# Optimization experiments

Measured on AMD Instinct MI355X. Metric: run time of the kernel, lower is better.

Reference implementation:

```python
import jax, jax.numpy as jnp
from jax import lax
import numpy as np

NDIM = 256
BATCH = 65536
NROT = NDIM * (NDIM - 1) // 2  # comb(ndim, 2) = 32640


def _givens_mat(rots, ii, jj, ndim):
    """Product G_last @ ... @ G_1 of Givens rotations in combinations order.

    Left-multiplying by G(i, j, theta) only modifies rows i and j, so we apply
    each rotation as a rank-2 row update instead of a full matmul (same math
    as the original `plane_rot_mat @ mat` loop).
    """
    def step(mat, carry):
        i, j, th = carry
        c = jnp.cos(th)
        s = jnp.sin(th)
        ri = mat[i]
        rj = mat[j]
        mat = mat.at[i].set(c * ri - s * rj)
        mat = mat.at[j].set(s * ri + c * rj)
        return mat, None

    mat0 = jnp.eye(ndim, dtype=jnp.complex64)
    mat, _ = lax.scan(step, mat0, (ii, jj, rots))
    return mat


def setup_inputs() -> dict:
    key = jax.random.key(0)
    k1, k2, k3, k4 = jax.random.split(key, 4)
    x = jax.random.normal(k1, (BATCH, NDIM), dtype=jnp.float32)
    rots1 = 0.1 * jax.random.normal(k2, (NROT,), dtype=jnp.float32)
    phases = 0.1 * jax.random.normal(k3, (NDIM,), dtype=jnp.float32)
    rots2 = 0.1 * jax.random.normal(k4, (NROT,), dtype=jnp.float32)
    return {"x": x, "rots1": rots1, "phases": phases, "rots2": rots2}


def reference(x, rots1, phases, rots2):
    ndim = x.shape[1]
    # np.triu_indices(ndim, 1) enumerates (i, j) pairs in the same row-major
    # order as itertools.combinations(range(ndim), 2).
    ii_np, jj_np = np.triu_indices(ndim, k=1)
    ii = jnp.asarray(ii_np, dtype=jnp.int32)
    jj = jnp.asarray(jj_np, dtype=jnp.int32)

    # vector_norm: row-wise L2 normalization
    xn = x / jnp.linalg.norm(x, axis=1, keepdims=True)
    xc = xn.astype(jnp.complex64)

    # rot1: y = x @ M1.T with M1 = G_last @ ... @ G_1
    M1 = _givens_mat(rots1, ii, jj, ndim)
    y = xc @ M1.T

    # phase_transforms: x @ diag(exp(i*phases)) == elementwise phase multiply
    y = y * jnp.exp(1j * phases)

    # rot2
    M2 = _givens_mat(rots2, ii, jj, ndim)
    y = y @ M2.T

    # measure: |.|^2
    return jnp.abs(y) ** 2
```

## Files before the change

### kernel.cpp

```cpp
#include <hip/hip_runtime.h>
#include <stdint.h>
#include <math.h>

#define NDIM 256
#define BATCH 65536
#define NROT 32640

typedef float  f32x4 __attribute__((ext_vector_type(4)));
typedef short  s16x8 __attribute__((ext_vector_type(8)));
typedef unsigned int u32x4 __attribute__((ext_vector_type(4)));
typedef unsigned int u32x2 __attribute__((ext_vector_type(2)));

static __device__ __forceinline__ unsigned short f2bf(float f) {
    unsigned int u = __float_as_uint(f);
    u += 0x7fffu + ((u >> 16) & 1u);
    return (unsigned short)(u >> 16);
}
static __device__ __forceinline__ float bf2f(unsigned short h) {
    return __uint_as_float(((unsigned)h) << 16);
}

static __device__ __forceinline__ void split4(f32x4 v, u32x2* hi, u32x2* lo) {
    unsigned short h[4], l[4];
    #pragma unroll
    for (int i = 0; i < 4; i++) {
        h[i] = f2bf(v[i]);
        l[i] = f2bf(v[i] - bf2f(h[i]));
    }
    *hi = (u32x2){ (unsigned)h[0] | ((unsigned)h[1] << 16),
                   (unsigned)h[2] | ((unsigned)h[3] << 16) };
    *lo = (u32x2){ (unsigned)l[0] | ((unsigned)l[1] << 16),
                   (unsigned)l[2] | ((unsigned)l[3] << 16) };
}
static __device__ __forceinline__ void split8(const float* v, u32x4* hi, u32x4* lo) {
    unsigned short h[8], l[8];
    #pragma unroll
    for (int i = 0; i < 8; i++) {
        h[i] = f2bf(v[i]);
        l[i] = f2bf(v[i] - bf2f(h[i]));
    }
    *hi = (u32x4){ (unsigned)h[0] | ((unsigned)h[1] << 16),
                   (unsigned)h[2] | ((unsigned)h[3] << 16),
                   (unsigned)h[4] | ((unsigned)h[5] << 16),
                   (unsigned)h[6] | ((unsigned)h[7] << 16) };
    *lo = (u32x4){ (unsigned)l[0] | ((unsigned)l[1] << 16),
                   (unsigned)l[2] | ((unsigned)l[3] << 16),
                   (unsigned)l[4] | ((unsigned)l[5] << 16),
                   (unsigned)l[6] | ((unsigned)l[7] << 16) };
}

static __device__ __forceinline__ int sweep_bound(int k, int pblk) {
    int target = k * (NROT / pblk);
    int best = 0, bd = 0x7fffffff;
    for (int i = 0; i <= 256; i += 4) {
        int pre = i * 255 - (i * (i - 1)) / 2;
        int d = pre - target; d = (d < 0) ? -d : d;
        if (d < bd) { bd = d; best = i; }
    }
    return best;
}

__global__ __launch_bounds__(256) void k_cs(const float* __restrict__ r1,
                                            const float* __restrict__ r2,
                                            float2* __restrict__ cs) {
    int i = blockIdx.x * 256 + threadIdx.x;
    float th = (i < NROT) ? r1[i] : r2[i - NROT];
    float sv, cv; sincosf(th, &sv, &cv);
    cs[i] = make_float2(cv, sv);
}

__global__ __launch_bounds__(64) void k_blocks(const float2* __restrict__ cs,
                                               float* __restrict__ bmats, int pblk) {
    __shared__ float colb[264 * 64];
    __shared__ float2 csb[256 * 4];
    __shared__ float2 tri[24 * 6];

    const int t = threadIdx.x;
    const int bid = blockIdx.x;
    const int chunk = bid & 3;
    const int b = (bid >> 2) % pblk;
    const int set = (bid >> 2) / pblk;
    const int col0 = chunk * 64;
    const float2* cst = cs + (size_t)set * NROT;

    const int s0 = sweep_bound(b, pblk);
    const int s1 = sweep_bound(b + 1, pblk);
    const int ngroups = (s1 - s0) >> 2;

    {
        const f32x4 z = {0.f, 0.f, 0.f, 0.f};
        #pragma unroll 11
        for (int q = 0; q < 66; q++)
            *(f32x4*)&colb[(q * 64 + t) * 4] = z;
        colb[(col0 + t) * 64 + t] = 1.0f;
    }

    for (int k = t; k < ngroups * 6; k += 64) {
        int g = k / 6, q = k - g * 6;
        int a  = (q < 3) ? 0 : ((q < 5) ? 1 : 2);
        int bb = (q < 3) ? (q + 1) : ((q < 5) ? (q - 1) : 3);
        int m0 = s0 + g * 4;
        int m = m0 + a;
        int base = m * 255 - (m * (m - 1)) / 2;
        tri[k] = cst[base - m - 1 + m0 + bb];
    }

    float2 gv[16];
    {
        const int m0g = s0;
        int offg[4];
        #pragma unroll
        for (int a = 0; a < 4; a++) {
            int m = m0g + a;
            offg[a] = m * 255 - (m * (m - 1)) / 2 - m - 1;
        }
        #pragma unroll
        for (int it = 0; it < 16; it++) {
            int k = t + it * 64;
            int jj = k >> 2, a = k & 3;
            int j = m0g + 4 + jj;
            gv[it] = (j < 256) ? cst[offg[a] + j] : make_float2(1.f, 0.f);
        }
        #pragma unroll
        for (int it = 0; it < 16; it++)
            csb[t + it * 64] = gv[it];
    }

    for (int g = 0; g < ngroups; g++) {
        const int m0 = s0 + g * 4;
        const int n_j = 252 - m0;
        const int n_p = (n_j > 0) ? ((n_j + 7) & ~7) : 0;
        const float* csbuf = (const float*)&csb[0];

        const bool have_next = (g + 1 < ngroups);
        if (have_next) {
            const int m0g = m0 + 4;
            int offg[4];
            #pragma unroll
            for (int a = 0; a < 4; a++) {
                int m = m0g + a;
                offg[a] = m * 255 - (m * (m - 1)) / 2 - m - 1;
            }
            #pragma unroll
            for (int it = 0; it < 16; it++) {
                int k = t + it * 64;
                int jj = k >> 2, a = k & 3;
                int j = m0g + 4 + jj;
                gv[it] = (j < 256) ? cst[offg[a] + j] : make_float2(1.f, 0.f);
            }
        }

        float u0 = colb[(m0 + 0) * 64 + t];
        float u1 = colb[(m0 + 1) * 64 + t];
        float u2 = colb[(m0 + 2) * 64 + t];
        float u3 = colb[(m0 + 3) * 64 + t];

        {
            float2 cv; float nr;
            cv = tri[g * 6 + 0]; nr = cv.y * u0 + cv.x * u1; u0 = cv.x * u0 - cv.y * u1; u1 = nr;
            cv = tri[g * 6 + 1]; nr = cv.y * u0 + cv.x * u2; u0 = cv.x * u0 - cv.y * u2; u2 = nr;
            cv = tri[g * 6 + 2]; nr = cv.y * u0 + cv.x * u3; u0 = cv.x * u0 - cv.y * u3; u3 = nr;
            cv = tri[g * 6 + 3]; nr = cv.y * u1 + cv.x * u2; u1 = cv.x * u1 - cv.y * u2; u2 = nr;
            cv = tri[g * 6 + 4]; nr = cv.y * u1 + cv.x * u3; u1 = cv.x * u1 - cv.y * u3; u3 = nr;
            cv = tri[g * 6 + 5]; nr = cv.y * u2 + cv.x * u3; u2 = cv.x * u2 - cv.y * u3; u3 = nr;
        }

        if (n_p > 0) {
            float rbuf[8];
            f32x4 abuf[8][2];
            #pragma unroll
            for (int p = 0; p < 8; p++) {
                rbuf[p] = colb[(m0 + 4 + p) * 64 + t];
                abuf[p][0] = *(const f32x4*)&csbuf[p * 8 + 0];
                abuf[p][1] = *(const f32x4*)&csbuf[p * 8 + 4];
            }
            for (int c = 0; c < n_p; c += 8) {
                #pragma unroll
                for (int p = 0; p < 8; p++) {
                    const int j = m0 + 4 + c + p;
                    float r = rbuf[p];
                    f32x4 A01 = abuf[p][0], A23 = abuf[p][1];
                    int jn = j + 8; jn = (jn < 263) ? jn : 263;
                    int cn = c + p + 8; cn = (cn < n_p) ? cn : (n_p - 1);
                    rbuf[p] = colb[jn * 64 + t];
                    abuf[p][0] = *(const f32x4*)&csbuf[cn * 8 + 0];
                    abuf[p][1] = *(const f32x4*)&csbuf[cn * 8 + 4];
                    float nr;
                    nr = A01[1] * u0 + A01[0] * r; u0 = A01[0] * u0 - A01[1] * r; r = nr;
                    nr = A01[3] * u1 + A01[2] * r; u1 = A01[2] * u1 - A01[3] * r; r = nr;
                    nr = A23[1] * u2 + A23[0] * r; u2 = A23[0] * u2 - A23[1] * r; r = nr;
                    nr = A23[3] * u3 + A23[2] * r; u3 = A23[2] * u3 - A23[3] * r; r = nr;
                    colb[j * 64 + t] = r;
                }
            }
        }
        colb[(m0 + 0) * 64 + t] = u0;
        colb[(m0 + 1) * 64 + t] = u1;
        colb[(m0 + 2) * 64 + t] = u2;
        colb[(m0 + 3) * 64 + t] = u3;

        if (have_next) {
            #pragma unroll
            for (int it = 0; it < 16; it++)
                csb[t + it * 64] = gv[it];
        }
    }

    float* outm = bmats + (size_t)(set * pblk + b) * 65536;
    for (int r = 0; r < 256; r++)
        outm[(size_t)r * 256 + col0 + t] = colb[r * 64 + t];
}

static __device__ __forceinline__ void xnorm_item(const float* __restrict__ xg,
                                                  unsigned short* __restrict__ xbf,
                                                  int id, int tid) {
    const int w = tid >> 6, lane = tid & 63;
    const int r0 = id * 64;
    #pragma unroll 2
    for (int p = 0; p < 16; p++) {
        int row = r0 + p * 4 + w;
        f32x4 v = *(const f32x4*)&xg[(size_t)row * 256 + lane * 4];
        float s = v[0] * v[0] + v[1] * v[1] + v[2] * v[2] + v[3] * v[3];
        #pragma unroll
        for (int off = 32; off; off >>= 1) s += __shfl_xor(s, off, 64);
        float sc = 1.0f / sqrtf(s);
        unsigned short h0 = f2bf(v[0] * sc), h1 = f2bf(v[1] * sc);
        unsigned short h2 = f2bf(v[2] * sc), h3 = f2bf(v[3] * sc);
        u32x2 pk = { (unsigned)h0 | ((unsigned)h1 << 16),
                     (unsigned)h2 | ((unsigned)h3 << 16) };
        *(u32x2*)&xbf[(size_t)row * 256 + lane * 4] = pk;
    }
}

#define TB 2560

static __device__ __forceinline__ int bslot(int row, int s) {
    return row * 40 + ((s ^ ((row >> 3) & 3)) << 3);
}

static __device__ __forceinline__ void tile_issueA(const float* __restrict__ Am,
                                                   int tr, int kb, int tid,
                                                   f32x4 va[2]) {
    #pragma unroll
    for (int it = 0; it < 2; it++) {
        int flat = tid + it * 256;
        int r = flat >> 3, c4 = flat & 7;
        va[it] = *(const f32x4*)&Am[(size_t)(tr * 64 + r) * 256 + kb * 32 + c4 * 4];
    }
}
static __device__ __forceinline__ void tile_issueB(const float* __restrict__ Bm,
                                                   int tc, int kb, int bn, int bkq,
                                                   float vb[8]) {
    #pragma unroll
    for (int i = 0; i < 8; i++)
        vb[i] = Bm[(size_t)(kb * 32 + bkq * 8 + i) * 256 + tc * 64 + bn];
}
static __device__ __forceinline__ void tile_commit(unsigned short* __restrict__ Ahi,
                                                   unsigned short* __restrict__ Alo,
                                                   unsigned short* __restrict__ Bhi,
                                                   unsigned short* __restrict__ Blo,
                                                   int tid, int bn, int bkq,
                                                   const f32x4 va[2], const float vb[8]) {
    #pragma unroll
    for (int it = 0; it < 2; it++) {
        int flat = tid + it * 256;
        int r = flat >> 3, c4 = flat & 7;
        u32x2 hi, lo; split4(va[it], &hi, &lo);
        *(u32x2*)&Ahi[r * 40 + c4 * 4] = hi;
        *(u32x2*)&Alo[r * 40 + c4 * 4] = lo;
    }
    u32x4 hi8, lo8; split8(vb, &hi8, &lo8);
    *(u32x4*)&Bhi[bslot(bn, bkq)] = hi8;
    *(u32x4*)&Blo[bslot(bn, bkq)] = lo8;
}
static __device__ __forceinline__ void tile_mfma(const unsigned short* __restrict__ Ahi,
                                                 const unsigned short* __restrict__ Alo,
                                                 const unsigned short* __restrict__ Bhi,
                                                 const unsigned short* __restrict__ Blo,
                                                 int mh, int nh, int l15, int lq,
                                                 f32x4 acc[2][2]) {
    s16x8 ah[2], al[2], bh[2], bl[2];
    #pragma unroll
    for (int tm = 0; tm < 2; tm++) {
        ah[tm] = *(const s16x8*)&Ahi[(mh + tm * 16 + l15) * 40 + lq * 8];
        al[tm] = *(const s16x8*)&Alo[(mh + tm * 16 + l15) * 40 + lq * 8];
    }
    #pragma unroll
    for (int tn = 0; tn < 2; tn++) {
        bh[tn] = *(const s16x8*)&Bhi[bslot(nh + tn * 16 + l15, lq)];
        bl[tn] = *(const s16x8*)&Blo[bslot(nh + tn * 16 + l15, lq)];
    }
    #pragma unroll
    for (int tm = 0; tm < 2; tm++)
        #pragma unroll
        for (int tn = 0; tn < 2; tn++) {
            acc[tm][tn] = __builtin_amdgcn_mfma_f32_16x16x32_bf16(ah[tm], bh[tn], acc[tm][tn], 0, 0, 0);
            acc[tm][tn] = __builtin_amdgcn_mfma_f32_16x16x32_bf16(ah[tm], bl[tn], acc[tm][tn], 0, 0, 0);
            acc[tm][tn] = __builtin_amdgcn_mfma_f32_16x16x32_bf16(al[tm], bh[tn], acc[tm][tn], 0, 0, 0);
        }
}

static __device__ void combine_tile(const float* __restrict__ src,
                                    float* __restrict__ dst,
                                    int half, int pblk, int bx, int by, int tid,
                                    unsigned short* Ahi, unsigned short* Alo,
                                    unsigned short* Bhi, unsigned short* Blo) {
    const int set = by / half, pidx = by % half;
    const int stride = pblk / (2 * half);
    const int s0A = sweep_bound((2 * pidx + 1) * stride, pblk);
    const float* Am = src + (size_t)(set * 2 * half + 2 * pidx + 1) * 65536;
    const float* Bm = src + (size_t)(set * 2 * half + 2 * pidx) * 65536;
    float* Dm = dst + (size_t)(set * half + pidx) * 65536;
    const int tr = bx >> 2, tc = bx & 3;

    if (tr * 64 + 64 <= s0A) {
        #pragma unroll
        for (int it = 0; it < 4; it++) {
            int flat = tid + it * 256;
            int r = flat >> 4, c4 = flat & 15;
            size_t idx = (size_t)(tr * 64 + r) * 256 + tc * 64 + c4 * 4;
            *(f32x4*)&Dm[idx] = *(const f32x4*)&Bm[idx];
        }
        return;
    }
    const int kb0 = (tr * 64 >= s0A) ? (s0A >> 5) : 0;

    const int lane = tid & 63, w = tid >> 6;
    const int mh = (w >> 1) * 32, nh = (w & 1) * 32;
    const int l15 = lane & 15, lq = lane >> 4;
    const int bn = tid & 63, bkq = tid >> 6;

    f32x4 acc[2][2];
    #pragma unroll
    for (int i = 0; i < 2; i++)
        #pragma unroll
        for (int j = 0; j < 2; j++) acc[i][j] = (f32x4){0.f, 0.f, 0.f, 0.f};

    f32x4 vaE[2], vaO[2]; float vbE[8], vbO[8];
    tile_issueA(Am, tr, kb0, tid, vaE);
    tile_issueB(Bm, tc, kb0, bn, bkq, vbE);
    if (kb0 + 1 < 8) {
        tile_issueA(Am, tr, kb0 + 1, tid, vaO);
        tile_issueB(Bm, tc, kb0 + 1, bn, bkq, vbO);
    }

    for (int kb = kb0; kb < 8; kb++) {
        const int cur = (kb - kb0) & 1;
        if (cur == 0) {
            tile_commit(Ahi, Alo, Bhi, Blo, tid, bn, bkq, vaE, vbE);
            __syncthreads();
            if (kb + 2 < 8) {
                tile_issueA(Am, tr, kb + 2, tid, vaE);
                tile_issueB(Bm, tc, kb + 2, bn, bkq, vbE);
            }
        } else {
            tile_commit(Ahi, Alo, Bhi, Blo, tid, bn, bkq, vaO, vbO);
            __syncthreads();
            if (kb + 2 < 8) {
                tile_issueA(Am, tr, kb + 2, tid, vaO);
                tile_issueB(Bm, tc, kb + 2, bn, bkq, vbO);
            }
        }
        tile_mfma(Ahi, Alo, Bhi, Blo, mh, nh, l15, lq, acc);
        __syncthreads();
    }
    #pragma unroll
    for (int tm = 0; tm < 2; tm++)
        #pragma unroll
        for (int tn = 0; tn < 2; tn++)
            #pragma unroll
            for (int r = 0; r < 4; r++)
                Dm[(size_t)(tr * 64 + mh + tm * 16 + lq * 4 + r) * 256
                   + tc * 64 + nh + tn * 16 + l15] = acc[tm][tn][r];
}

__global__ __launch_bounds__(256) void k_combine(const float* __restrict__ src,
                                                 float* __restrict__ dst,
                                                 int half, int pblk,
                                                 const float* __restrict__ xg,
                                                 unsigned short* __restrict__ xbf) {
    __shared__ unsigned short Ahi[TB], Alo[TB], Bhi[TB], Blo[TB];
    const int by = blockIdx.y, tid = threadIdx.x;
    if (by >= 2 * half) {
        xnorm_item(xg, xbf, (by - 2 * half) * 16 + blockIdx.x, tid);
        return;
    }
    combine_tile(src, dst, half, pblk, blockIdx.x, by, tid, Ahi, Alo, Bhi, Blo);
}

__global__ __launch_bounds__(256) void k_abt_part(const float* __restrict__ mats,
                                                  const float* __restrict__ phases,
                                                  float* __restrict__ part) {
    __shared__ unsigned short Ahi[TB], Alo[TB], Bhi[TB], Blo[TB];
    const float* Am = mats + 65536;
    const float* Bm = mats;
    const int tid = threadIdx.x;
    const int bx = blockIdx.x;
    const int v  = blockIdx.y;
    const int kb = blockIdx.z;
    const int tr = bx >> 2, tc = bx & 3;

    const int lane = tid & 63, w = tid >> 6;
    const int mh = (w >> 1) * 32, nh = (w & 1) * 32;
    const int l15 = lane & 15, lq = lane >> 4;
    const int bn = tid & 63, bkq = tid >> 6;

    f32x4 va[2]; float vb[8];
    tile_issueA(Am, tr, kb, tid, va);
    #pragma unroll
    for (int i = 0; i < 8; i++) {
        int kg = kb * 32 + bkq * 8 + i;
        float ph = phases[kg];
        float sc = v ? sinf(ph) : cosf(ph);
        vb[i] = Bm[(size_t)kg * 256 + tc * 64 + bn] * sc;
    }

    f32x4 acc[2][2];
    #pragma unroll
    for (int i = 0; i < 2; i++)
        #pragma unroll
        for (int j = 0; j < 2; j++) acc[i][j] = (f32x4){0.f, 0.f, 0.f, 0.f};

    tile_commit(Ahi, Alo, Bhi, Blo, tid, bn, bkq, va, vb);
    __syncthreads();
    tile_mfma(Ahi, Alo, Bhi, Blo, mh, nh, l15, lq, acc);

    float* pp = part + (size_t)(kb * 2 + v) * 65536;
    #pragma unroll
    for (int tm = 0; tm < 2; tm++)
        #pragma unroll
        for (int tn = 0; tn < 2; tn++)
            #pragma unroll
            for (int r = 0; r < 4; r++)
                pp[(size_t)(tr * 64 + mh + tm * 16 + lq * 4 + r) * 256
                   + tc * 64 + nh + tn * 16 + l15] = acc[tm][tn][r];
}

__global__ __launch_bounds__(256) void k_abt_red(const float* __restrict__ part,
                                                 unsigned short* __restrict__ abt) {
    const int e = (blockIdx.x * 256 + threadIdx.x) * 4;
    f32x4 s = {0.f, 0.f, 0.f, 0.f};
    #pragma unroll
    for (int kz = 0; kz < 8; kz++)
        s += *(const f32x4*)&part[(size_t)kz * 131072 + e];
    unsigned short h0 = f2bf(s[0]), h1 = f2bf(s[1]);
    unsigned short h2 = f2bf(s[2]), h3 = f2bf(s[3]);
    u32x2 pk = { (unsigned)h0 | ((unsigned)h1 << 16),
                 (unsigned)h2 | ((unsigned)h3 << 16) };
    *(u32x2*)&abt[e] = pk;
}

__global__ __launch_bounds__(256) void k_norm(const float* __restrict__ x,
                                              float* __restrict__ invn) {
    const int row = blockIdx.x * 4 + (threadIdx.x >> 6);
    const int lane = threadIdx.x & 63;
    f32x4 v = *(const f32x4*)&x[(size_t)row * 256 + lane * 4];
    float s = v[0] * v[0] + v[1] * v[1] + v[2] * v[2] + v[3] * v[3];
    for (int off = 32; off; off >>= 1) s += __shfl_xor(s, off, 64);
    if (lane == 0) invn[row] = 1.0f / sqrtf(s);
}

#define BKP 136
__global__ __launch_bounds__(256) void k_gemm_bf(const unsigned short* __restrict__ xbf,
                                                 const unsigned short* __restrict__ abt,
                                                 float* __restrict__ out) {
    __shared__ unsigned short As[128 * BKP];
    __shared__ unsigned short Bs[128 * BKP];
    const int tid = threadIdx.x;
    const int l  = blockIdx.y * 4 + blockIdx.x;
    const int L  = (l & 7) * 256 + (l >> 3);
    const int cb = L & 3;
    const int rb = L >> 2;
    const int lane = tid & 63, w = tid >> 6;

    f32x4 acc[16];
    #pragma unroll
    for (int i = 0; i < 16; i++) acc[i] = (f32x4){0.f, 0.f, 0.f, 0.f};

    int rA[8], cA[8], grB[8];
    #pragma unroll
    for (int it = 0; it < 8; it++) {
        int flat = tid + it * 256;
        rA[it] = flat >> 4; cA[it] = flat & 15;
        int r = rA[it];
        grB[it] = (r < 64) ? (cb * 64 + r) : (256 + cb * 64 + (r - 64));
    }

    u32x4 pa[8], pb[8];
    #pragma unroll
    for (int it = 0; it < 8; it++) {
        pa[it] = *(const u32x4*)&xbf[(size_t)(rb * 128 + rA[it]) * 256 + cA[it] * 8];
        pb[it] = *(const u32x4*)&abt[(size_t)grB[it] * 256 + cA[it] * 8];
    }
    #pragma unroll
    for (int it = 0; it < 8; it++) {
        *(u32x4*)&As[rA[it] * BKP + cA[it] * 8] = pa[it];
        *(u32x4*)&Bs[rA[it] * BKP + cA[it] * 8] = pb[it];
    }
    __syncthreads();
    #pragma unroll
    for (int it = 0; it < 8; it++) {
        pa[it] = *(const u32x4*)&xbf[(size_t)(rb * 128 + rA[it]) * 256 + 128 + cA[it] * 8];
        pb[it] = *(const u32x4*)&abt[(size_t)grB[it] * 256 + 128 + cA[it] * 8];
    }

    auto compute = [&]() {
        #pragma unroll
        for (int ks = 0; ks < 4; ks++) {
            const int k0 = ks * 32 + (lane >> 4) * 8;
            s16x8 a[2], b[8];
            #pragma unroll
            for (int tm = 0; tm < 2; tm++)
                a[tm] = *(const s16x8*)&As[(w * 32 + tm * 16 + (lane & 15)) * BKP + k0];
            #pragma unroll
            for (int tn = 0; tn < 8; tn++)
                b[tn] = *(const s16x8*)&Bs[(tn * 16 + (lane & 15)) * BKP + k0];
            #pragma unroll
            for (int tm = 0; tm < 2; tm++)
                #pragma unroll
                for (int tn = 0; tn < 8; tn++)
                    acc[tm * 8 + tn] = __builtin_amdgcn_mfma_f32_16x16x32_bf16(
                        a[tm], b[tn], acc[tm * 8 + tn], 0, 0, 0);
        }
    };
    compute();
    __syncthreads();
    #pragma unroll
    for (int it = 0; it < 8; it++) {
        *(u32x4*)&As[rA[it] * BKP + cA[it] * 8] = pa[it];
        *(u32x4*)&Bs[rA[it] * BKP + cA[it] * 8] = pb[it];
    }
    __syncthreads();
    compute();

    const int qr = lane >> 4, c = lane & 15;
    #pragma unroll
    for (int tm = 0; tm < 2; tm++) {
        #pragma unroll
        for (int tn = 0; tn < 4; tn++) {
            f32x4 p = acc[tm * 8 + tn];
            f32x4 q = acc[tm * 8 + tn + 4];
            #pragma unroll
            for (int r = 0; r < 4; r++) {
                int m = w * 32 + tm * 16 + qr * 4 + r;
                out[(size_t)(rb * 128 + m) * 256 + cb * 64 + tn * 16 + c] =
                    p[r] * p[r] + q[r] * q[r];
            }
        }
    }
}

__global__ __launch_bounds__(256) void k_gemm_f32(const float* __restrict__ x,
                                                  const unsigned short* __restrict__ abt,
                                                  const float* __restrict__ invn,
                                                  float* __restrict__ out) {
    __shared__ unsigned short As[128 * BKP];
    __shared__ unsigned short Bs[128 * BKP];
    const int tid = threadIdx.x;
    const int l  = blockIdx.y * 4 + blockIdx.x;
    const int L  = (l & 7) * 256 + (l >> 3);
    const int cb = L & 3;
    const int rb = L >> 2;
    const int lane = tid & 63, w = tid >> 6;

    f32x4 acc[16];
    #pragma unroll
    for (int i = 0; i < 16; i++) acc[i] = (f32x4){0.f, 0.f, 0.f, 0.f};

    for (int kb = 0; kb < 2; kb++) {
        __syncthreads();
        #pragma unroll
        for (int it = 0; it < 16; it++) {
            int flat = tid + it * 256;
            int r = flat >> 5, c4 = flat & 31;
            f32x4 v = *(const f32x4*)&x[(size_t)(rb * 128 + r) * 256 + kb * 128 + c4 * 4];
            float sc = invn[rb * 128 + r];
            v[0] *= sc; v[1] *= sc; v[2] *= sc; v[3] *= sc;
            unsigned short h0 = f2bf(v[0]), h1 = f2bf(v[1]);
            unsigned short h2 = f2bf(v[2]), h3 = f2bf(v[3]);
            u32x2 pk = { (unsigned)h0 | ((unsigned)h1 << 16),
                         (unsigned)h2 | ((unsigned)h3 << 16) };
            *(u32x2*)&As[r * BKP + c4 * 4] = pk;
        }
        #pragma unroll
        for (int it = 0; it < 8; it++) {
            int flat = tid + it * 256;
            int r = flat >> 4, c8 = flat & 15;
            int gr = (r < 64) ? (cb * 64 + r) : (256 + cb * 64 + (r - 64));
            u32x4 vv = *(const u32x4*)&abt[(size_t)gr * 256 + kb * 128 + c8 * 8];
            *(u32x4*)&Bs[r * BKP + c8 * 8] = vv;
        }
        __syncthreads();
        #pragma unroll
        for (int ks = 0; ks < 4; ks++) {
            const int k0 = ks * 32 + (lane >> 4) * 8;
            s16x8 a[2], b[8];
            #pragma unroll
            for (int tm = 0; tm < 2; tm++)
                a[tm] = *(const s16x8*)&As[(w * 32 + tm * 16 + (lane & 15)) * BKP + k0];
            #pragma unroll
            for (int tn = 0; tn < 8; tn++)
                b[tn] = *(const s16x8*)&Bs[(tn * 16 + (lane & 15)) * BKP + k0];
            #pragma unroll
            for (int tm = 0; tm < 2; tm++)
                #pragma unroll
                for (int tn = 0; tn < 8; tn++)
                    acc[tm * 8 + tn] = __builtin_amdgcn_mfma_f32_16x16x32_bf16(
                        a[tm], b[tn], acc[tm * 8 + tn], 0, 0, 0);
        }
    }

    const int qr = lane >> 4, c = lane & 15;
    #pragma unroll
    for (int tm = 0; tm < 2; tm++) {
        #pragma unroll
        for (int tn = 0; tn < 4; tn++) {
            f32x4 p = acc[tm * 8 + tn];
            f32x4 q = acc[tm * 8 + tn + 4];
            #pragma unroll
            for (int r = 0; r < 4; r++) {
                int m = w * 32 + tm * 16 + qr * 4 + r;
                out[(size_t)(rb * 128 + m) * 256 + cb * 64 + tn * 16 + c] =
                    p[r] * p[r] + q[r] * q[r];
            }
        }
    }
}

extern "C" void kernel_launch(void* const* d_in, const int* in_sizes, int n_in,
                              void* d_out, int out_size, void* d_ws, size_t ws_size,
                              hipStream_t stream) {
    (void)in_sizes; (void)n_in; (void)out_size;
    const float* x      = (const float*)d_in[0];
    const float* rots1  = (const float*)d_in[1];
    const float* phases = (const float*)d_in[2];
    const float* rots2  = (const float*)d_in[3];
    float* out = (float*)d_out;
    char* ws = (char*)d_ws;

    const size_t MAT = 262144;
    int pblk = 64;
    while (pblk > 16 &&
           (size_t)3 * pblk * MAT + 2 * MAT + (size_t)BATCH * 512 > ws_size)
        pblk >>= 1;
    const size_t offA   = 0;
    const size_t offB   = offA + (size_t)2 * pblk * MAT;
    const size_t offABT = offB + (size_t)pblk * MAT;
    const size_t offINV = offABT + MAT;
    const size_t offXBF = offINV + MAT;
    const bool use_xbf = (offXBF + (size_t)BATCH * 512) <= ws_size;

    float*          A    = (float*)(ws + offA);
    float*          B    = (float*)(ws + offB);
    unsigned short* abt  = (unsigned short*)(ws + offABT);
    float*          invn = (float*)(ws + offINV);
    unsigned short* xbf  = (unsigned short*)(ws + offXBF);
    float2*         cs   = (float2*)(ws + offB);

    k_cs<<<(2 * NROT) / 256, 256, 0, stream>>>(rots1, rots2, cs);
    k_blocks<<<8 * pblk, 64, 0, stream>>>(cs, A, pblk);

    float* srcp = A; float* dstp = B;
    bool first = true;
    for (int half = pblk / 2; half >= 1; half >>= 1) {
        const int xny = (first && use_xbf) ? 64 : 0;
        k_combine<<<dim3(16, 2 * half + xny), 256, 0, stream>>>(srcp, dstp, half,
                                                                pblk, x, xbf);
        float* tmp = srcp; srcp = dstp; dstp = tmp;
        first = false;
    }
    k_abt_part<<<dim3(16, 2, 8), 256, 0, stream>>>(srcp, phases, dstp);
    k_abt_red<<<128, 256, 0, stream>>>(dstp, abt);

    if (use_xbf) {
        k_gemm_bf<<<dim3(4, BATCH / 128), 256, 0, stream>>>(xbf, abt, out);
    } else {
        k_norm<<<BATCH / 4, 256, 0, stream>>>(x, invn);
        k_gemm_f32<<<dim3(4, BATCH / 128), 256, 0, stream>>>(x, abt, invn, out);
    }
}
```

Before: 262.1 us.

## Move row normalization into spare waves of the Givens block kernel

The x row-normalization and bf16 conversion move out of the first combine launch and into the Givens block-building kernel. That kernel is widened from one wave to four per block, and the three extra waves stream rows of x while wave 0 does the serial rotation work. The aim is to hide the memory-bound normalization behind the latency-bound serial chain instead of lengthening the first combine step. The larger block size and the shared-memory footprint of k_blocks may limit occupancy, and the extra memory traffic could slow the serial waves.

```diff
diff --git a/kernel.cpp b/kernel.cpp
--- a/kernel.cpp
+++ b/kernel.cpp
@@ -69,14 +69,58 @@
     cs[i] = make_float2(cv, sv);
 }
 
-__global__ __launch_bounds__(64) void k_blocks(const float2* __restrict__ cs,
-                                               float* __restrict__ bmats, int pblk) {
+__global__ __launch_bounds__(256) void k_blocks(const float2* __restrict__ cs,
+                                                float* __restrict__ bmats, int pblk,
+                                                const float* __restrict__ xg,
+                                                unsigned short* __restrict__ xbf,
+                                                int do_xn) {
     __shared__ float colb[264 * 64];
     __shared__ float2 csb[256 * 4];
     __shared__ float2 tri[24 * 6];
 
-    const int t = threadIdx.x;
     const int bid = blockIdx.x;
+    const int wid = threadIdx.x >> 6;
+    const int lane = threadIdx.x & 63;
+
+    if (wid != 0) {
+        if (!do_xn) return;
+        const int W  = bid * 3 + (wid - 1);
+        const int nW = (int)gridDim.x * 3;
+        const int per = (BATCH + nW - 1) / nW;
+        int r0 = W * per;
+        int rend = r0 + per; if (rend > BATCH) rend = BATCH;
+        for (int row = r0; row < rend; row += 2) {
+            const bool has2 = (row + 1 < rend);
+            f32x4 v0 = *(const f32x4*)&xg[(size_t)row * 256 + lane * 4];
+            f32x4 v1 = has2 ? *(const f32x4*)&xg[(size_t)(row + 1) * 256 + lane * 4]
+                            : v0;
+            float s0 = v0[0] * v0[0] + v0[1] * v0[1] + v0[2] * v0[2] + v0[3] * v0[3];
+            float s1 = v1[0] * v1[0] + v1[1] * v1[1] + v1[2] * v1[2] + v1[3] * v1[3];
+            #pragma unroll
+            for (int off = 32; off; off >>= 1) {
+                s0 += __shfl_xor(s0, off, 64);
+                s1 += __shfl_xor(s1, off, 64);
+            }
+            float sc0 = 1.0f / sqrtf(s0), sc1 = 1.0f / sqrtf(s1);
+            {
+                unsigned short h0 = f2bf(v0[0] * sc0), h1 = f2bf(v0[1] * sc0);
+                unsigned short h2 = f2bf(v0[2] * sc0), h3 = f2bf(v0[3] * sc0);
+                u32x2 pk = { (unsigned)h0 | ((unsigned)h1 << 16),
+                             (unsigned)h2 | ((unsigned)h3 << 16) };
+                *(u32x2*)&xbf[(size_t)row * 256 + lane * 4] = pk;
+            }
+            if (has2) {
+                unsigned short h0 = f2bf(v1[0] * sc1), h1 = f2bf(v1[1] * sc1);
+                unsigned short h2 = f2bf(v1[2] * sc1), h3 = f2bf(v1[3] * sc1);
+                u32x2 pk = { (unsigned)h0 | ((unsigned)h1 << 16),
+                             (unsigned)h2 | ((unsigned)h3 << 16) };
+                *(u32x2*)&xbf[(size_t)(row + 1) * 256 + lane * 4] = pk;
+            }
+        }
+        return;
+    }
+
+    const int t = lane;
     const int chunk = bid & 3;
     const int b = (bid >> 2) % pblk;
     const int set = (bid >> 2) / pblk;
@@ -211,27 +255,6 @@
         outm[(size_t)r * 256 + col0 + t] = colb[r * 64 + t];
 }
 
-static __device__ __forceinline__ void xnorm_item(const float* __restrict__ xg,
-                                                  unsigned short* __restrict__ xbf,
-                                                  int id, int tid) {
-    const int w = tid >> 6, lane = tid & 63;
-    const int r0 = id * 64;
-    #pragma unroll 2
-    for (int p = 0; p < 16; p++) {
-        int row = r0 + p * 4 + w;
-        f32x4 v = *(const f32x4*)&xg[(size_t)row * 256 + lane * 4];
-        float s = v[0] * v[0] + v[1] * v[1] + v[2] * v[2] + v[3] * v[3];
-        #pragma unroll
-        for (int off = 32; off; off >>= 1) s += __shfl_xor(s, off, 64);
-        float sc = 1.0f / sqrtf(s);
-        unsigned short h0 = f2bf(v[0] * sc), h1 = f2bf(v[1] * sc);
-        unsigned short h2 = f2bf(v[2] * sc), h3 = f2bf(v[3] * sc);
-        u32x2 pk = { (unsigned)h0 | ((unsigned)h1 << 16),
-                     (unsigned)h2 | ((unsigned)h3 << 16) };
-        *(u32x2*)&xbf[(size_t)row * 256 + lane * 4] = pk;
-    }
-}
-
 #define TB 2560
 
 static __device__ __forceinline__ int bslot(int row, int s) {
@@ -376,16 +399,10 @@
 
 __global__ __launch_bounds__(256) void k_combine(const float* __restrict__ src,
                                                  float* __restrict__ dst,
-                                                 int half, int pblk,
-                                                 const float* __restrict__ xg,
-                                                 unsigned short* __restrict__ xbf) {
+                                                 int half, int pblk) {
     __shared__ unsigned short Ahi[TB], Alo[TB], Bhi[TB], Blo[TB];
-    const int by = blockIdx.y, tid = threadIdx.x;
-    if (by >= 2 * half) {
-        xnorm_item(xg, xbf, (by - 2 * half) * 16 + blockIdx.x, tid);
-        return;
-    }
-    combine_tile(src, dst, half, pblk, blockIdx.x, by, tid, Ahi, Alo, Bhi, Blo);
+    combine_tile(src, dst, half, pblk, blockIdx.x, blockIdx.y, threadIdx.x,
+                 Ahi, Alo, Bhi, Blo);
 }
 
 __global__ __launch_bounds__(256) void k_abt_part(const float* __restrict__ mats,
@@ -658,16 +675,12 @@
     float2*         cs   = (float2*)(ws + offB);
 
     k_cs<<<(2 * NROT) / 256, 256, 0, stream>>>(rots1, rots2, cs);
-    k_blocks<<<8 * pblk, 64, 0, stream>>>(cs, A, pblk);
+    k_blocks<<<8 * pblk, 256, 0, stream>>>(cs, A, pblk, x, xbf, use_xbf ? 1 : 0);
 
     float* srcp = A; float* dstp = B;
-    bool first = true;
     for (int half = pblk / 2; half >= 1; half >>= 1) {
-        const int xny = (first && use_xbf) ? 64 : 0;
-        k_combine<<<dim3(16, 2 * half + xny), 256, 0, stream>>>(srcp, dstp, half,
-                                                                pblk, x, xbf);
+        k_combine<<<dim3(16, 2 * half), 256, 0, stream>>>(srcp, dstp, half, pblk);
         float* tmp = srcp; srcp = dstp; dstp = tmp;
-        first = false;
     }
     k_abt_part<<<dim3(16, 2, 8), 256, 0, stream>>>(srcp, phases, dstp);
     k_abt_red<<<128, 256, 0, stream>>>(dstp, abt);
```

Result: no change. 261.5 us (-0.2%).
